# Kernel tuning notes

Measured on AMD Instinct MI355X. Metric: run time of the kernel, lower is better.

The kernel has to match this reference:

```python
import jax, jax.numpy as jnp
import numpy as np

B, N = 16384, 20
F = 128          # n_node_features = n_neighbors_features = embed_dim
T = 100          # time_dim
E = 128          # n_edge_features
H = 2            # n_head
OUT = 128        # output_dimension
KEY_DIM = F + T + E  # 356


def setup_inputs() -> dict:
    key = jax.random.key(0)
    ks = jax.random.split(key, 24)
    s = 0.02
    inp = {
        "src_node_features": jax.random.normal(ks[0], (B, F), jnp.float32),
        "neighbors_features": jax.random.normal(ks[1], (B, N, F), jnp.float32),
        "neighbors_time_features": jax.random.normal(ks[2], (B, N, T), jnp.float32),
        "edge_features": jax.random.normal(ks[3], (B, N, E), jnp.float32),
        "neighbors_padding_mask": jax.random.randint(ks[4], (B, N), 0, 2).astype(bool),
        "weights": jax.random.uniform(ks[5], (B, N), jnp.float32),
        # transform: Linear(key_dim -> F)
        "Wt": jax.random.normal(ks[6], (F, KEY_DIM), jnp.float32) * s,
        "bt": jnp.zeros((F,), jnp.float32),
        # MultiheadAttention projections (embed_dim = kdim = vdim = F)
        "Wq": jax.random.normal(ks[7], (F, F), jnp.float32) * s,
        "bq": jnp.zeros((F,), jnp.float32),
        "Wk": jax.random.normal(ks[8], (F, F), jnp.float32) * s,
        "bk": jnp.zeros((F,), jnp.float32),
        "Wv": jax.random.normal(ks[9], (F, F), jnp.float32) * s,
        "bv": jnp.zeros((F,), jnp.float32),
        "Wo": jax.random.normal(ks[10], (F, F), jnp.float32) * s,
        "bo": jnp.zeros((F,), jnp.float32),
        # MergeLayer: fc1(query_dim + F -> F), fc2(F -> OUT)
        "W1": jax.random.normal(ks[11], (F, F + F), jnp.float32) * s,
        "b1": jnp.zeros((F,), jnp.float32),
        "W2": jax.random.normal(ks[12], (OUT, F), jnp.float32) * s,
        "b2": jnp.zeros((OUT,), jnp.float32),
    }
    return inp


def _gat_forward(src, nbr, timef, edgef, w, mask,
                 Wt, bt, Wq, bq, Wk, bk, Wv, bv, Wo, bo, W1, b1, W2, b2):
    b, f = src.shape
    dh = f // H
    scale = 1.0 / jnp.sqrt(jnp.asarray(dh, src.dtype))
    # key = transform(cat([nbr, edge, time])) * weights  -> [B,N,F]
    k_in = jnp.concatenate([nbr, edgef, timef], axis=2)
    keyv = (jnp.einsum('bnk,fk->bnf', k_in, Wt) + bt) * w[:, :, None]
    # invalid-neighborhood fixup: rows fully padded get their first slot unmasked
    invalid = mask.all(axis=1, keepdims=True)           # [B,1]
    mask = mask.at[:, 0].set(jnp.where(invalid[:, 0], False, mask[:, 0]))
    # projections (query_len = 1)
    q = (src @ Wq.T + bq).reshape(b, H, dh)             # [B,H,dh]
    k = (keyv @ Wk.T + bk).reshape(b, N, H, dh)         # [B,N,H,dh]
    v = (keyv @ Wv.T + bv).reshape(b, N, H, dh)
    scores = jnp.einsum('bhd,bnhd->bhn', q, k) * scale  # [B,H,N]
    scores = jnp.where(mask[:, None, :], -jnp.inf, scores)
    attn = jax.nn.softmax(scores, axis=-1)
    ctx = jnp.einsum('bhn,bnhd->bhd', attn, v).reshape(b, f)
    out = ctx @ Wo.T + bo                               # [B,F]
    out = jnp.where(invalid, jnp.asarray(0.0, out.dtype), out)
    out = jax.nn.relu(out)
    # MergeLayer: fc2(relu(fc1(cat([attn_out, src]))))
    hmid = jax.nn.relu(jnp.concatenate([out, src], axis=1) @ W1.T + b1)
    return hmid @ W2.T + b2


def reference(src_node_features, neighbors_features, neighbors_time_features,
              edge_features, neighbors_padding_mask, weights,
              Wt, bt, Wq, bq, Wk, bk, Wv, bv, Wo, bo, W1, b1, W2, b2):
    return _gat_forward(src_node_features, neighbors_features,
                        neighbors_time_features, edge_features, weights,
                        neighbors_padding_mask,
                        Wt, bt, Wq, bq, Wk, bk, Wv, bv, Wo, bo, W1, b1, W2, b2)
```

## Files before the change

kernel.cpp:

```cpp
#include <hip/hip_runtime.h>
#include <math.h>

#define NN 20
#define FF 128
#define TT 100
#define EE 128
#define KD 356

typedef unsigned int u32;
typedef unsigned short u16;
typedef unsigned long long u64;
typedef __attribute__((ext_vector_type(4))) float f32x4;
typedef __attribute__((ext_vector_type(8))) short s16x8;
typedef __attribute__((ext_vector_type(4))) u32 u32x4;

__device__ __forceinline__ u16 f2b(float f) {
    u32 u = __float_as_uint(f);
    u32 r = u + 0x7FFFu + ((u >> 16) & 1u);
    return (u16)(r >> 16);
}
__device__ __forceinline__ float b2f(u16 h) { return __uint_as_float(((u32)h) << 16); }
__device__ __forceinline__ float blo(u32 u){ return __uint_as_float(u << 16); }
__device__ __forceinline__ float bhi(u32 u){ return __uint_as_float(u & 0xFFFF0000u); }
__device__ __forceinline__ u32 pk2(float a, float b){ return (u32)f2b(a) | ((u32)f2b(b) << 16); }
__device__ __forceinline__ u32 cvtpk(float a, float b){
    u32 d; asm("v_cvt_pk_bf16_f32 %0, %1, %2" : "=v"(d) : "v"(a), "v"(b)); return d;
}


__global__ void prep_fuse(const float* __restrict__ Wt, const float* __restrict__ bt,
                          const float* __restrict__ Wk, const float* __restrict__ Wv,
                          const u32* __restrict__ maskw,
                          float* __restrict__ wkt, float* __restrict__ wvt,
                          float* __restrict__ kfb, float* __restrict__ vfb, int* __restrict__ flagp)
{
    const int blk = blockIdx.x, t = threadIdx.x;
    if (blk < KD) {
        __shared__ float col[FF];
        col[t] = Wt[t * KD + blk];
        __syncthreads();
        float ak = 0.f, av = 0.f;
        for (int j = 0; j < FF; ++j) {
            float c = col[j];
            ak = fmaf(Wk[t * FF + j], c, ak);
            av = fmaf(Wv[t * FF + j], c, av);
        }
        wkt[blk * FF + t] = ak;
        wvt[blk * FF + t] = av;
    } else if (blk == KD) {
        float ak = 0.f, av = 0.f;
        for (int j = 0; j < FF; ++j) {
            float c = bt[j];
            ak = fmaf(Wk[t * FF + j], c, ak);
            av = fmaf(Wv[t * FF + j], c, av);
        }
        kfb[t] = ak; vfb[t] = av;
    } else {
        int any = 0;
        for (int i = t; i < 8192; i += 128) any |= (maskw[i] > 1u) ? 1 : 0;
        any = __any(any) ? 1 : 0;
        __shared__ int red[2];
        if ((t & 63) == 0) red[t >> 6] = any;
        __syncthreads();
        if (t == 0) *flagp = (red[0] | red[1]) ? 1 : 0;
    }
}

__global__ void prep_pack_v4(const float* __restrict__ wkt, const float* __restrict__ wvt,
                             const float* __restrict__ Wq, const float* __restrict__ Wo,
                             const float* __restrict__ W1, const float* __restrict__ W2,
                             u16* __restrict__ kvB, u16* __restrict__ wqI, u16* __restrict__ woI,
                             u16* __restrict__ w1I, u16* __restrict__ w2I)
{
    const int id = blockIdx.x * 256 + threadIdx.x;
    if (id < 196608) {
        int chunk = id >> 9, e = id & 511;
        int ln = e >> 3, ee = e & 7;
        int kt = chunk >> 4, nb = chunk & 15;
        int k = kt * 32 + (ln >> 4) * 8 + ee;
        int n = nb * 16 + (ln & 15);
        float v = 0.f;
        if (k < KD) v = (n < FF) ? wkt[k * FF + n] : wvt[k * FF + (n - FF)];
        kvB[id] = f2b(v);
    } else if (id < 215040) {
        int e = id - 196608; int rem = e % 9216;
        int n = rem / 72, kk = rem % 72; int k = (e / 9216) * 64 + kk;
        wqI[e] = f2b(kk < 64 ? Wq[n * FF + k] : 0.f);
    } else if (id < 233472) {
        int e = id - 215040; int rem = e % 9216;
        int n = rem / 72, kk = rem % 72; int k = (e / 9216) * 64 + kk;
        woI[e] = f2b(kk < 64 ? Wo[n * FF + k] : 0.f);
    } else if (id < 270336) {
        int e = id - 233472; int rem = e % 9216;
        int n = rem / 72, kk = rem % 72; int k = (e / 9216) * 64 + kk;
        w1I[e] = f2b(kk < 64 ? W1[n * 2 * FF + k] : 0.f);
    } else if (id < 288768) {
        int e = id - 270336; int rem = e % 9216;
        int n = rem / 72, kk = rem % 72; int k = (e / 9216) * 64 + kk;
        w2I[e] = f2b(kk < 64 ? W2[n * FF + k] : 0.f);
    }
}

__global__ __launch_bounds__(512) void kv_attn_fused7(
    const float* __restrict__ nbr, const float* __restrict__ edg, const float* __restrict__ tmf,
    const float* __restrict__ wgt, const float* __restrict__ bk, const float* __restrict__ bv,
    const u16* __restrict__ kvB, const float* __restrict__ kfb, const float* __restrict__ vfb,
    const u16* __restrict__ Qg, const void* __restrict__ maskp, const int* __restrict__ flagp,
    u16* __restrict__ ctxout, unsigned char* __restrict__ flags)
{
    __shared__ __align__(16) u16 smem[15680];
    char* sb = (char*)smem;
    float* p_lds = (float*)(sb + 30720);
    u16* kls = (u16*)sb;

    const int tid = threadIdx.x;
    const int lane = tid & 63, wave = tid >> 6;
    const int wn = wave;
    const int Mbase = blockIdx.x * 80;
    const int Bbase = blockIdx.x * 4;
    const int kg = lane >> 4, l16 = lane & 15;

    f32x4 acc[5][2] = {};
    s16x8 br[2][2];
    f32x4 tl[5];

    #define STAGE_CHUNK(C, KT) do {                                                         \
        int row_ = (C) * 8 + (lane >> 3);                                                   \
        int x_ = (lane & 7) ^ (row_ & 7);                                                   \
        const float* g_;                                                                    \
        if ((KT) < 4)      g_ = nbr + (size_t)(Mbase + row_) * 128 + (KT) * 32 + x_ * 4;    \
        else if ((KT) < 8) g_ = edg + (size_t)(Mbase + row_) * 128 + ((KT)-4) * 32 + x_ * 4;\
        else               g_ = tmf + (size_t)(Mbase + row_) * 100 + ((KT)-8) * 32 + x_ * 4;\
        __builtin_amdgcn_global_load_lds((const __attribute__((address_space(1))) u32*)g_,  \
            (__attribute__((address_space(3))) u32*)(sb + ((KT)%3)*10240 + (C)*1024), 16, 0, 0); \
    } while (0)

    #define STAGE(KT) do {                                                                  \
        STAGE_CHUNK(wave, KT);                                                              \
        if (wave < 2) STAGE_CHUNK(8 + wave, KT);                                            \
    } while (0)

    #define LOADB(KT) do {                                                                  \
        br[(KT)&1][0] = *(const s16x8*)(kvB + (size_t)((KT)*16 + wn*2 + 0)*512 + lane*8);   \
        br[(KT)&1][1] = *(const s16x8*)(kvB + (size_t)((KT)*16 + wn*2 + 1)*512 + lane*8);   \
    } while (0)

    #define NV1(KT) ((KT)==0?6:((KT)==1?8:((KT)==2?10:((KT)<=8?8:((KT)==9?7:6)))))
    #define NV2(KT) ((KT)==0?8:((KT)==1?10:((KT)==2?12:((KT)<=8?10:((KT)==9?8:6)))))

    #pragma unroll
    for (int mt = 0; mt < 5; ++mt)
        tl[mt] = *(const f32x4*)(tmf + (size_t)(Mbase + mt * 16 + l16) * 100 + 96);
    STAGE(0); STAGE(1); STAGE(2);
    LOADB(0); LOADB(1);

    #define GITER(KT) do {                                                                  \
        if ((KT) <= 10) {                                                                   \
            if (wave < 2) { asm volatile("s_waitcnt vmcnt(%0)" :: "i"(NV2(KT)) : "memory"); }\
            else          { asm volatile("s_waitcnt vmcnt(%0)" :: "i"(NV1(KT)) : "memory"); }\
            __builtin_amdgcn_s_barrier();                                                   \
            __builtin_amdgcn_sched_barrier(0);                                              \
        }                                                                                   \
        s16x8 af[5];                                                                        \
        _Pragma("unroll")                                                                   \
        for (int mt = 0; mt < 5; ++mt) {                                                    \
            f32x4 lo, hi;                                                                   \
            if ((KT) <= 10) {                                                               \
                int r_ = mt * 16 + l16; int sw_ = r_ & 7; int y0_ = kg * 2;                 \
                const char* bp_ = sb + ((KT)%3)*10240 + r_ * 128;                           \
                lo = *(const f32x4*)(bp_ + ((y0_ ^ sw_) << 4));                             \
                hi = *(const f32x4*)(bp_ + (((y0_+1) ^ sw_) << 4));                         \
            } else {                                                                        \
                lo = (kg == 0) ? tl[mt] : (f32x4){0.f,0.f,0.f,0.f};                         \
                hi = (f32x4){0.f,0.f,0.f,0.f};                                              \
            }                                                                               \
            u32x4 q_;                                                                       \
            q_.x = cvtpk(lo.x, lo.y); q_.y = cvtpk(lo.z, lo.w);                             \
            q_.z = cvtpk(hi.x, hi.y); q_.w = cvtpk(hi.z, hi.w);                             \
            af[mt] = __builtin_bit_cast(s16x8, q_);                                         \
        }                                                                                   \
        _Pragma("unroll")                                                                   \
        for (int mt = 0; mt < 5; ++mt) {                                                    \
            acc[mt][0] = __builtin_amdgcn_mfma_f32_16x16x32_bf16(af[mt], br[(KT)&1][0], acc[mt][0], 0, 0, 0); \
            acc[mt][1] = __builtin_amdgcn_mfma_f32_16x16x32_bf16(af[mt], br[(KT)&1][1], acc[mt][1], 0, 0, 0); \
        }                                                                                   \
        if ((KT) <= 10) {                                                                   \
            asm volatile("s_waitcnt lgkmcnt(0)" ::: "memory");                              \
            __builtin_amdgcn_s_barrier();                                                   \
            __builtin_amdgcn_sched_barrier(0);                                              \
            if ((KT) <= 7) STAGE((KT)+3);                                                   \
            if ((KT)+2 <= 11) LOADB((KT)+2);                                                \
        }                                                                                   \
    } while (0)

    GITER(0); GITER(1); GITER(2);  GITER(3);
    GITER(4); GITER(5); GITER(6);  GITER(7);
    GITER(8); GITER(9); GITER(10); GITER(11);
    #undef GITER
    #undef STAGE
    #undef STAGE_CHUNK
    #undef LOADB

    __syncthreads();

    const int rg4 = (lane >> 4) * 4;
    if (wn < 4) {
        #pragma unroll
        for (int mt = 0; mt < 5; ++mt) {
            const int r0 = mt * 16 + rg4;
            float w4v[4];
            #pragma unroll
            for (int i = 0; i < 4; ++i) w4v[i] = wgt[Mbase + r0 + i];
            #pragma unroll
            for (int nt = 0; nt < 2; ++nt) {
                const int c = wn * 32 + nt * 16 + l16;
                const float fb = kfb[c], bb = bk[c];
                #pragma unroll
                for (int i = 0; i < 4; ++i)
                    kls[(r0 + i) * 132 + c] = f2b(fmaf(acc[mt][nt][i] + fb, w4v[i], bb));
            }
        }
    } else {
        #pragma unroll
        for (int mt = 0; mt < 5; ++mt) {
            const int r0 = mt * 16 + rg4;
            float w4v[4];
            #pragma unroll
            for (int i = 0; i < 4; ++i) w4v[i] = wgt[Mbase + r0 + i];
            #pragma unroll
            for (int nt = 0; nt < 2; ++nt) {
                const int c = (wn - 4) * 32 + nt * 16 + l16;
                const float fb = vfb[c], bb = bv[c];
                #pragma unroll
                for (int i = 0; i < 4; ++i)
                    acc[mt][nt][i] = fmaf(acc[mt][nt][i] + fb, w4v[i], bb);
            }
        }
    }
    __syncthreads();

    const int lb = wave >> 1, h = wave & 1;
    const int brow = Bbase + lb;
    {
        const int flagv = *flagp;
        bool mybit = false;
        if (lane < NN) {
            if (flagv) mybit = ((const unsigned char*)maskp)[brow * NN + lane] != 0;
            else       mybit = ((const int*)maskp)[brow * NN + lane] != 0;
        }
        u64 bal = __ballot(mybit);
        u32 mb = (u32)(bal & 0xFFFFFull);
        const bool invalid = (mb == 0xFFFFFu);
        if (invalid) mb &= ~1u;
        if (h == 0 && lane == 0) flags[brow] = invalid ? 1 : 0;

        const int n = lane & 31;
        float s = -INFINITY;
        if (lane < 32 && n < NN) {
            const u16* kr = kls + (lb * NN + n) * 132 + h * 64;
            const u16* qr = Qg + (size_t)brow * 128 + h * 64;
            float d = 0.f;
            #pragma unroll
            for (int dc = 0; dc < 16; ++dc) {
                uint2 kw = *(const uint2*)(kr + dc * 4);
                uint2 qw = *(const uint2*)(qr + dc * 4);
                d = fmaf(blo(kw.x), blo(qw.x), d);  d = fmaf(bhi(kw.x), bhi(qw.x), d);
                d = fmaf(blo(kw.y), blo(qw.y), d);  d = fmaf(bhi(kw.y), bhi(qw.y), d);
            }
            s = ((mb >> n) & 1u) ? -INFINITY : d * 0.125f;
        }
        float mx = s;
        #pragma unroll
        for (int off = 16; off; off >>= 1) mx = fmaxf(mx, __shfl_xor(mx, off, 32));
        float e = (lane < 32 && n < NN) ? expf(s - mx) : 0.f;
        float sum = e;
        #pragma unroll
        for (int off = 16; off; off >>= 1) sum += __shfl_xor(sum, off, 32);
        if (lane < NN) p_lds[wave * NN + lane] = e / sum;
    }
    __syncthreads();

    if (wn >= 4) {
        #pragma unroll
        for (int mt = 0; mt < 5; ++mt) {
            const int r0 = mt * 16 + rg4;
            #pragma unroll
            for (int nt = 0; nt < 2; ++nt) {
                const int c = (wn - 4) * 32 + nt * 16 + l16;
                #pragma unroll
                for (int i = 0; i < 4; ++i)
                    kls[(r0 + i) * 132 + c] = f2b(acc[mt][nt][i]);
            }
        }
    }
    __syncthreads();

    {
        float cacc = 0.f;
        #pragma unroll
        for (int n2 = 0; n2 < NN; ++n2) {
            float pn = p_lds[wave * NN + n2];
            cacc = fmaf(pn, b2f(kls[(lb * NN + n2) * 132 + h * 64 + lane]), cacc);
        }
        ctxout[(size_t)brow * 128 + h * 64 + lane] = f2b(cacc);
    }
}

#define GM_Q 0
#define GM_O 1
#define GM_H 2
#define GM_F 3

template<int MODE>
__global__ __launch_bounds__(256) void gemm_small(
    const void* __restrict__ Asrc, const float* __restrict__ Asrc2,
    const u16* __restrict__ Bimg, const float* __restrict__ bias,
    const unsigned char* __restrict__ flags, void* __restrict__ outp)
{
    __shared__ u16 lA[64 * 72];
    __shared__ u16 lB[128 * 72];
    const int tid = threadIdx.x;
    const int Mbase = blockIdx.x * 64;
    const int lane = tid & 63, wave = tid >> 6;
    const int wm = wave >> 1, wn = wave & 1;
    const int row = tid >> 2, cg = tid & 3;

    constexpr int KTILES = (MODE == GM_H) ? 4 : 2;
    f32x4 acc[2][4] = {};
    const size_t r = (size_t)(Mbase + row);

    for (int kt = 0; kt < KTILES; ++kt) {
        if (MODE == GM_Q || (MODE == GM_H && kt >= 2)) {
            const float* ap = (MODE == GM_Q)
                ? ((const float*)Asrc + r * 128 + kt * 64 + cg * 16)
                : (Asrc2 + r * 128 + (kt - 2) * 64 + cg * 16);
            f32x4 x0 = *(const f32x4*)ap,       x1 = *(const f32x4*)(ap + 4);
            f32x4 x2 = *(const f32x4*)(ap + 8), x3 = *(const f32x4*)(ap + 12);
            *(uint4*)(&lA[row * 72 + cg * 16])     = make_uint4(pk2(x0.x,x0.y), pk2(x0.z,x0.w), pk2(x1.x,x1.y), pk2(x1.z,x1.w));
            *(uint4*)(&lA[row * 72 + cg * 16 + 8]) = make_uint4(pk2(x2.x,x2.y), pk2(x2.z,x2.w), pk2(x3.x,x3.y), pk2(x3.z,x3.w));
        } else {
            const u16* ap = (const u16*)Asrc + r * 128 + kt * 64 + cg * 16;
            *(uint4*)(&lA[row * 72 + cg * 16])     = *(const uint4*)ap;
            *(uint4*)(&lA[row * 72 + cg * 16 + 8]) = *(const uint4*)(ap + 8);
        }
        for (int c = wave; c < 18; c += 4) {
            const char* g = (const char*)Bimg + (size_t)kt * 18432 + c * 1024 + lane * 16;
            char* l = (char*)lB + c * 1024;
            __builtin_amdgcn_global_load_lds((const __attribute__((address_space(1))) u32*)g,
                                             (__attribute__((address_space(3))) u32*)l, 16, 0, 0);
        }
        __syncthreads();
        #pragma unroll
        for (int ks = 0; ks < 2; ++ks) {
            int kk = ks * 32 + (lane >> 4) * 8;
            s16x8 a[2], b[4];
            #pragma unroll
            for (int mt = 0; mt < 2; ++mt)
                a[mt] = *(const s16x8*)(&lA[(wm * 32 + mt * 16 + (lane & 15)) * 72 + kk]);
            #pragma unroll
            for (int nt = 0; nt < 4; ++nt)
                b[nt] = *(const s16x8*)(&lB[(wn * 64 + nt * 16 + (lane & 15)) * 72 + kk]);
            #pragma unroll
            for (int mt = 0; mt < 2; ++mt)
                #pragma unroll
                for (int nt = 0; nt < 4; ++nt)
                    acc[mt][nt] = __builtin_amdgcn_mfma_f32_16x16x32_bf16(a[mt], b[nt], acc[mt][nt], 0, 0, 0);
        }
        __syncthreads();
    }

    #pragma unroll
    for (int mt = 0; mt < 2; ++mt) {
        #pragma unroll
        for (int nt = 0; nt < 4; ++nt) {
            int colg = wn * 64 + nt * 16 + (lane & 15);
            float bb = bias[colg];
            #pragma unroll
            for (int i = 0; i < 4; ++i) {
                int rg = Mbase + wm * 32 + mt * 16 + (lane >> 4) * 4 + i;
                float val = acc[mt][nt][i] + bb;
                if (MODE == GM_O) { if (flags[rg]) val = 0.f; val = fmaxf(val, 0.f); }
                if (MODE == GM_H) val = fmaxf(val, 0.f);
                if (MODE == GM_F) ((float*)outp)[(size_t)rg * 128 + colg] = val;
                else              ((u16*)outp)[(size_t)rg * 128 + colg] = f2b(val);
            }
        }
    }
}


__global__ void prep_pack_r2(const float* __restrict__ wkt, const float* __restrict__ wvt,
                             const float* __restrict__ Wq, const float* __restrict__ Wo,
                             const float* __restrict__ W1, const float* __restrict__ W2,
                             u16* __restrict__ bpack, u32* __restrict__ wq2, u32* __restrict__ wo2,
                             u32* __restrict__ w12, u32* __restrict__ w22)
{
    const int id = blockIdx.x * 256 + threadIdx.x;
    if (id < 98304) {
        int kt = id >> 14;
        int o  = id & 16383;
        int n  = o >> 6;
        int kk = (o & 63) ^ ((n & 7) << 3);
        int k  = kt * 64 + kk;
        float v = 0.f;
        if (k < KD) v = (n < FF) ? wkt[k * FF + n] : wvt[k * FF + (n - FF)];
        bpack[id] = f2b(v);
    } else if (id < 106496) {
        int e = id - 98304; int j = e >> 6, tt = e & 63;
        wq2[e] = (u32)f2b(Wq[tt * FF + j]) | ((u32)f2b(Wq[(tt + 64) * FF + j]) << 16);
    } else if (id < 114688) {
        int e = id - 106496; int j = e >> 6, tt = e & 63;
        wo2[e] = (u32)f2b(Wo[tt * FF + j]) | ((u32)f2b(Wo[(tt + 64) * FF + j]) << 16);
    } else if (id < 131072) {
        int e = id - 114688; int j = e >> 6, tt = e & 63;
        w12[e] = (u32)f2b(W1[tt * 2 * FF + j]) | ((u32)f2b(W1[(tt + 64) * 2 * FF + j]) << 16);
    } else if (id < 139264) {
        int e = id - 131072; int j = e >> 6, tt = e & 63;
        w22[e] = (u32)f2b(W2[tt * FF + j]) | ((u32)f2b(W2[(tt + 64) * FF + j]) << 16);
    }
}

__global__ __launch_bounds__(512) void kv_gemm_r2(
    const float* __restrict__ nbr, const float* __restrict__ edg, const float* __restrict__ tmf,
    const float* __restrict__ wgt, const float* __restrict__ bk, const float* __restrict__ bv,
    const u16* __restrict__ bpack, const float* __restrict__ kfb, const float* __restrict__ vfb,
    u16* __restrict__ kvout)
{
    __shared__ u16 lA[128 * 64];
    __shared__ u16 lB[256 * 64];
    const int tid = threadIdx.x;
    const int Mbase = blockIdx.x * 128;
    const int lane = tid & 63, wave = tid >> 6;
    const int wm = wave >> 2, wn = wave & 3;

    f32x4 acc[4][4] = {};
    const int rq = tid >> 4;
    const int cq = tid & 15;

    for (int kt = 0; kt < 6; ++kt) {
        #pragma unroll
        for (int i = 0; i < 4; ++i) {
            int row = rq + i * 32;
            size_t r = (size_t)(Mbase + row);
            f32x4 v;
            if (kt < 2)       v = *(const f32x4*)(nbr + r * 128 + kt * 64 + cq * 4);
            else if (kt < 4)  v = *(const f32x4*)(edg + r * 128 + (kt - 2) * 64 + cq * 4);
            else if (kt == 4) v = *(const f32x4*)(tmf + r * 100 + cq * 4);
            else if (cq < 9)  v = *(const f32x4*)(tmf + r * 100 + 64 + cq * 4);
            else              v = (f32x4){0.f, 0.f, 0.f, 0.f};
            int off = row * 64 + ((cq * 4) ^ ((row & 7) << 3));
            *(uint2*)(&lA[off]) = make_uint2(pk2(v.x, v.y), pk2(v.z, v.w));
        }
        #pragma unroll
        for (int i = 0; i < 4; ++i) {
            int boff = wave * 4096 + i * 1024;
            const char* g = (const char*)bpack + (size_t)kt * 32768 + boff + lane * 16;
            char* l = (char*)lB + boff;
            __builtin_amdgcn_global_load_lds((const __attribute__((address_space(1))) u32*)g,
                                             (__attribute__((address_space(3))) u32*)l, 16, 0, 0);
        }
        __syncthreads();
        #pragma unroll
        for (int ks = 0; ks < 2; ++ks) {
            int kk = ks * 32 + (lane >> 4) * 8;
            s16x8 a[4], b[4];
            #pragma unroll
            for (int mt = 0; mt < 4; ++mt) {
                int m = wm * 64 + mt * 16 + (lane & 15);
                a[mt] = *(const s16x8*)(&lA[m * 64 + (kk ^ ((m & 7) << 3))]);
            }
            #pragma unroll
            for (int nt = 0; nt < 4; ++nt) {
                int n = wn * 64 + nt * 16 + (lane & 15);
                b[nt] = *(const s16x8*)(&lB[n * 64 + (kk ^ ((n & 7) << 3))]);
            }
            #pragma unroll
            for (int mt = 0; mt < 4; ++mt)
                #pragma unroll
                for (int nt = 0; nt < 4; ++nt)
                    acc[mt][nt] = __builtin_amdgcn_mfma_f32_16x16x32_bf16(a[mt], b[nt], acc[mt][nt], 0, 0, 0);
        }
        __syncthreads();
    }

    #pragma unroll
    for (int mt = 0; mt < 4; ++mt) {
        float w4[4];
        #pragma unroll
        for (int i = 0; i < 4; ++i)
            w4[i] = wgt[Mbase + wm * 64 + mt * 16 + (lane >> 4) * 4 + i];
        #pragma unroll
        for (int nt = 0; nt < 4; ++nt) {
            int c = wn * 64 + nt * 16 + (lane & 15);
            float fb   = (c < FF) ? kfb[c] : vfb[c - FF];
            float bias = (c < FF) ? bk[c]  : bv[c - FF];
            #pragma unroll
            for (int i = 0; i < 4; ++i) {
                int rr = Mbase + wm * 64 + mt * 16 + (lane >> 4) * 4 + i;
                float val = fmaf(acc[mt][nt][i] + fb, w4[i], bias);
                kvout[(size_t)rr * 256 + c] = f2b(val);
            }
        }
    }
}

__global__ __launch_bounds__(64) void gat_attn_r2(
    const float* __restrict__ src, const void* __restrict__ maskp,
    const float* __restrict__ bq, const float* __restrict__ bo,
    const float* __restrict__ b1, const float* __restrict__ b2,
    const u16* __restrict__ kv, const u32* __restrict__ wq2, const u32* __restrict__ wo2,
    const u32* __restrict__ w12, const u32* __restrict__ w22,
    const int* __restrict__ flagp, float* __restrict__ out)
{
    const int b = blockIdx.x, t = threadIdx.x;
    __shared__ u16 kls[NN * 132];
    __shared__ float s_src[FF], s_q[FF], s_ctx[FF], s_out[FF], s_h[FF];
    __shared__ float s_sc[2 * NN];

    const int flag = *flagp;
    bool mybit = false;
    if (t < NN) {
        if (flag) mybit = ((const unsigned char*)maskp)[b * NN + t] != 0;
        else      mybit = ((const int*)maskp)[b * NN + t] != 0;
    }
    u64 bal = __ballot(mybit);
    u32 mb = (u32)(bal & 0xFFFFFull);
    const bool invalid = (mb == 0xFFFFFu);
    if (invalid) mb &= ~1u;

    s_src[t] = src[(size_t)b * FF + t];
    s_src[t + 64] = src[(size_t)b * FF + 64 + t];

    float v0[NN], v1[NN];
    #pragma unroll
    for (int n = 0; n < NN; ++n) {
        const u16* row = kv + ((size_t)b * NN + n) * 256;
        kls[n * 132 + t]      = row[t];
        kls[n * 132 + 64 + t] = row[64 + t];
        v0[n] = b2f(row[128 + t]);
        v1[n] = b2f(row[192 + t]);
    }
    __syncthreads();

    {
        float q0 = bq[t], q1 = bq[64 + t];
        for (int j = 0; j < FF; ++j) {
            u32 u = wq2[j * 64 + t];
            float sj = s_src[j];
            q0 = fmaf(blo(u), sj, q0);
            q1 = fmaf(bhi(u), sj, q1);
        }
        s_q[t] = q0; s_q[64 + t] = q1;
    }
    __syncthreads();

    if (t < 2 * NN) {
        int h = t / NN, n = t - (t / NN) * NN;
        const u16* kr = kls + n * 132 + h * 64;
        const float* qr = s_q + h * 64;
        float s = 0.f;
        #pragma unroll
        for (int d = 0; d < 64; ++d) s = fmaf(qr[d], b2f(kr[d]), s);
        s *= 0.125f;
        s_sc[t] = ((mb >> n) & 1u) ? -INFINITY : s;
    }
    __syncthreads();
    if (t < 2) {
        float mx = -INFINITY;
        for (int n = 0; n < NN; ++n) mx = fmaxf(mx, s_sc[t * NN + n]);
        float e[NN]; float sum = 0.f;
        for (int n = 0; n < NN; ++n) { e[n] = expf(s_sc[t * NN + n] - mx); sum += e[n]; }
        float inv = 1.f / sum;
        for (int n = 0; n < NN; ++n) s_sc[t * NN + n] = e[n] * inv;
    }
    __syncthreads();

    {
        float c0 = 0.f, c1 = 0.f;
        #pragma unroll
        for (int n = 0; n < NN; ++n) {
            c0 = fmaf(s_sc[n],      v0[n], c0);
            c1 = fmaf(s_sc[NN + n], v1[n], c1);
        }
        s_ctx[t] = c0; s_ctx[64 + t] = c1;
    }
    __syncthreads();

    {
        float o0 = bo[t], o1 = bo[64 + t];
        for (int j = 0; j < FF; ++j) {
            u32 u = wo2[j * 64 + t];
            float cj = s_ctx[j];
            o0 = fmaf(blo(u), cj, o0);
            o1 = fmaf(bhi(u), cj, o1);
        }
        if (invalid) { o0 = 0.f; o1 = 0.f; }
        o0 = fmaxf(o0, 0.f); o1 = fmaxf(o1, 0.f);
        s_out[t] = o0; s_out[64 + t] = o1;
    }
    __syncthreads();

    {
        float h0 = b1[t], h1 = b1[64 + t];
        for (int j = 0; j < FF; ++j) {
            u32 u = w12[j * 64 + t];
            float xj = s_out[j];
            h0 = fmaf(blo(u), xj, h0);
            h1 = fmaf(bhi(u), xj, h1);
        }
        for (int j = 0; j < FF; ++j) {
            u32 u = w12[(FF + j) * 64 + t];
            float xj = s_src[j];
            h0 = fmaf(blo(u), xj, h0);
            h1 = fmaf(bhi(u), xj, h1);
        }
        h0 = fmaxf(h0, 0.f); h1 = fmaxf(h1, 0.f);
        s_h[t] = h0; s_h[64 + t] = h1;
    }
    __syncthreads();

    {
        float f0 = b2[t], f1 = b2[64 + t];
        for (int j = 0; j < FF; ++j) {
            u32 u = w22[j * 64 + t];
            float hj = s_h[j];
            f0 = fmaf(blo(u), hj, f0);
            f1 = fmaf(bhi(u), hj, f1);
        }
        out[(size_t)b * FF + t] = f0;
        out[(size_t)b * FF + 64 + t] = f1;
    }
}


#define FB_WKT  0
#define FB_WVT  (FB_WKT + KD*FF)
#define FB_KB   (FB_WVT + KD*FF)
#define FB_VB   (FB_KB + FF)
#define FB_WQT  (FB_VB + FF)
#define FB_WOT  (FB_WQT + FF*FF)
#define FB_W1T  (FB_WOT + FF*FF)
#define FB_W2T  (FB_W1T + 2*FF*FF)
#define FB_FLAG (FB_W2T + FF*FF)

__global__ void gat_prep_fb(const float* __restrict__ Wt, const float* __restrict__ bt,
                            const float* __restrict__ Wq, const float* __restrict__ Wk,
                            const float* __restrict__ Wv, const float* __restrict__ Wo,
                            const float* __restrict__ W1, const float* __restrict__ W2,
                            const u32* __restrict__ maskw, float* __restrict__ ws)
{
    const int blk = blockIdx.x;
    const int t = threadIdx.x;
    if (blk < KD) {
        __shared__ float col[FF];
        col[t] = Wt[t * KD + blk];
        __syncthreads();
        float ak = 0.f, av = 0.f;
        for (int j = 0; j < FF; ++j) {
            float c = col[j];
            ak = fmaf(Wk[t * FF + j], c, ak);
            av = fmaf(Wv[t * FF + j], c, av);
        }
        ws[FB_WKT + blk * FF + t] = ak;
        ws[FB_WVT + blk * FF + t] = av;
    } else if (blk == KD) {
        float ak = 0.f, av = 0.f;
        for (int j = 0; j < FF; ++j) {
            float c = bt[j];
            ak = fmaf(Wk[t * FF + j], c, ak);
            av = fmaf(Wv[t * FF + j], c, av);
        }
        ws[FB_KB + t] = ak;
        ws[FB_VB + t] = av;
    } else if (blk == KD + 1) {
        int any = 0;
        for (int i = t; i < 8192; i += 128) any |= (maskw[i] > 1u) ? 1 : 0;
        any = __any(any) ? 1 : 0;
        __shared__ int red[2];
        if ((t & 63) == 0) red[t >> 6] = any;
        __syncthreads();
        if (t == 0) ((int*)ws)[FB_FLAG] = (red[0] | red[1]) ? 1 : 0;
    } else {
        int id = (blk - (KD + 2)) * 128 + t;
        if (id < FF * FF) {
            int k = id >> 7, f = id & 127;
            ws[FB_WQT + id] = Wq[f * FF + k];
        } else if (id < 2 * FF * FF) {
            int e = id - FF * FF; int k = e >> 7, f = e & 127;
            ws[FB_WOT + e] = Wo[f * FF + k];
        } else if (id < 4 * FF * FF) {
            int e = id - 2 * FF * FF; int j = e >> 7, f = e & 127;
            ws[FB_W1T + e] = W1[f * (2 * FF) + j];
        } else if (id < 5 * FF * FF) {
            int e = id - 4 * FF * FF; int k = e >> 7, f = e & 127;
            ws[FB_W2T + e] = W2[f * FF + k];
        }
    }
}

__global__ __launch_bounds__(64) void gat_main_fb(
    const float* __restrict__ src, const float* __restrict__ nbr,
    const float* __restrict__ tmf, const float* __restrict__ edg,
    const void* __restrict__ maskp, const float* __restrict__ wgt,
    const float* __restrict__ bq, const float* __restrict__ bk,
    const float* __restrict__ bv, const float* __restrict__ bo,
    const float* __restrict__ b1, const float* __restrict__ b2,
    const float* __restrict__ ws, float* __restrict__ out)
{
    const int b = blockIdx.x;
    const int t = threadIdx.x;
    __shared__ __align__(16) float kin[KD * NN];
    __shared__ float s_src[FF], s_q[FF], s_ctx[FF], s_out[FF], s_h[FF];
    __shared__ float s_w[NN], s_sc[2 * NN];

    const int flag = ((const int*)ws)[FB_FLAG];
    bool mybit = false;
    if (t < NN) {
        if (flag) mybit = ((const unsigned char*)maskp)[b * NN + t] != 0;
        else      mybit = ((const int*)maskp)[b * NN + t] != 0;
    }
    u64 bal = __ballot(mybit);
    u32 mb = (u32)(bal & 0xFFFFFull);
    const bool invalid = (mb == 0xFFFFFu);
    if (invalid) mb &= ~1u;

    s_src[t] = src[(size_t)b * FF + t];
    s_src[t + 64] = src[(size_t)b * FF + 64 + t];
    if (t < NN) s_w[t] = wgt[(size_t)b * NN + t];

    for (int idx = t; idx < NN * FF; idx += 64) {
        int n = idx >> 7, j = idx & 127;
        kin[j * NN + n]         = nbr[((size_t)b * NN + n) * FF + j];
        kin[(128 + j) * NN + n] = edg[((size_t)b * NN + n) * EE + j];
    }
    for (int idx = t; idx < NN * TT; idx += 64) {
        int n = idx / TT, j = idx - n * TT;
        kin[(256 + j) * NN + n] = tmf[((size_t)b * NN + n) * TT + j];
    }
    __syncthreads();

    const float* wkt = ws + FB_WKT;
    const float* wvt = ws + FB_WVT;
    float ak0[NN], ak1[NN], av0[NN], av1[NN];
#pragma unroll
    for (int n = 0; n < NN; ++n) { ak0[n] = 0.f; ak1[n] = 0.f; av0[n] = 0.f; av1[n] = 0.f; }
    for (int k = 0; k < KD; ++k) {
        float wk0 = wkt[k * FF + t],      wk1 = wkt[k * FF + 64 + t];
        float wv0 = wvt[k * FF + t],      wv1 = wvt[k * FF + 64 + t];
        const float4* cp = (const float4*)(kin + k * NN);
        float4 ca = cp[0], cb = cp[1], cc = cp[2], cd = cp[3], ce = cp[4];
        const float c[NN] = { ca.x, ca.y, ca.z, ca.w,  cb.x, cb.y, cb.z, cb.w,
                              cc.x, cc.y, cc.z, cc.w,  cd.x, cd.y, cd.z, cd.w,
                              ce.x, ce.y, ce.z, ce.w };
#pragma unroll
        for (int n = 0; n < NN; ++n) {
            ak0[n] = fmaf(wk0, c[n], ak0[n]);
            ak1[n] = fmaf(wk1, c[n], ak1[n]);
            av0[n] = fmaf(wv0, c[n], av0[n]);
            av1[n] = fmaf(wv1, c[n], av1[n]);
        }
    }
    __syncthreads();

    float* kls = kin;
    float* vls = kin + NN * 129;
    {
        const float kb0 = ws[FB_KB + t], kb1 = ws[FB_KB + 64 + t];
        const float vb0 = ws[FB_VB + t], vb1 = ws[FB_VB + 64 + t];
        const float k0b = bk[t], k1b = bk[64 + t];
        const float v0b = bv[t], v1b = bv[64 + t];
#pragma unroll
        for (int n = 0; n < NN; ++n) {
            float wn = s_w[n];
            kls[n * 129 + t]      = fmaf(wn, ak0[n] + kb0, k0b);
            kls[n * 129 + 64 + t] = fmaf(wn, ak1[n] + kb1, k1b);
            vls[n * 129 + t]      = fmaf(wn, av0[n] + vb0, v0b);
            vls[n * 129 + 64 + t] = fmaf(wn, av1[n] + vb1, v1b);
        }
    }
    {
        const float* wqT = ws + FB_WQT;
        float q0 = bq[t], q1 = bq[64 + t];
        for (int j = 0; j < FF; ++j) {
            float sj = s_src[j];
            q0 = fmaf(wqT[j * FF + t], sj, q0);
            q1 = fmaf(wqT[j * FF + 64 + t], sj, q1);
        }
        s_q[t] = q0; s_q[64 + t] = q1;
    }
    __syncthreads();

    if (t < 2 * NN) {
        int h = t / NN, n = t - (t / NN) * NN;
        const float* kr = kls + n * 129 + h * 64;
        const float* qr = s_q + h * 64;
        float s = 0.f;
#pragma unroll
        for (int d = 0; d < 64; ++d) s = fmaf(qr[d], kr[d], s);
        s *= 0.125f;
        s_sc[t] = ((mb >> n) & 1u) ? -INFINITY : s;
    }
    __syncthreads();
    if (t < 2) {
        float mx = -INFINITY;
        for (int n = 0; n < NN; ++n) mx = fmaxf(mx, s_sc[t * NN + n]);
        float e[NN]; float sum = 0.f;
        for (int n = 0; n < NN; ++n) { e[n] = expf(s_sc[t * NN + n] - mx); sum += e[n]; }
        float inv = 1.f / sum;
        for (int n = 0; n < NN; ++n) s_sc[t * NN + n] = e[n] * inv;
    }
    __syncthreads();

    {
        float c0 = 0.f, c1 = 0.f;
#pragma unroll
        for (int n = 0; n < NN; ++n) {
            c0 = fmaf(s_sc[n],      vls[n * 129 + t],      c0);
            c1 = fmaf(s_sc[NN + n], vls[n * 129 + 64 + t], c1);
        }
        s_ctx[t] = c0; s_ctx[64 + t] = c1;
    }
    __syncthreads();

    {
        const float* woT = ws + FB_WOT;
        float o0 = bo[t], o1 = bo[64 + t];
        for (int j = 0; j < FF; ++j) {
            float cj = s_ctx[j];
            o0 = fmaf(woT[j * FF + t], cj, o0);
            o1 = fmaf(woT[j * FF + 64 + t], cj, o1);
        }
        if (invalid) { o0 = 0.f; o1 = 0.f; }
        o0 = fmaxf(o0, 0.f); o1 = fmaxf(o1, 0.f);
        s_out[t] = o0; s_out[64 + t] = o1;
    }
    __syncthreads();

    {
        const float* w1T = ws + FB_W1T;
        float h0 = b1[t], h1 = b1[64 + t];
        for (int j = 0; j < FF; ++j) {
            float xj = s_out[j];
            h0 = fmaf(w1T[j * FF + t], xj, h0);
            h1 = fmaf(w1T[j * FF + 64 + t], xj, h1);
        }
        for (int j = 0; j < FF; ++j) {
            float xj = s_src[j];
            h0 = fmaf(w1T[(FF + j) * FF + t], xj, h0);
            h1 = fmaf(w1T[(FF + j) * FF + 64 + t], xj, h1);
        }
        h0 = fmaxf(h0, 0.f); h1 = fmaxf(h1, 0.f);
        s_h[t] = h0; s_h[64 + t] = h1;
    }
    __syncthreads();

    {
        const float* w2T = ws + FB_W2T;
        float f0 = b2[t], f1 = b2[64 + t];
        for (int j = 0; j < FF; ++j) {
            float hj = s_h[j];
            f0 = fmaf(w2T[j * FF + t], hj, f0);
            f1 = fmaf(w2T[j * FF + 64 + t], hj, f1);
        }
        out[(size_t)b * FF + t] = f0;
        out[(size_t)b * FF + 64 + t] = f1;
    }
}


extern "C" void kernel_launch(void* const* d_in, const int* in_sizes, int n_in,
                              void* d_out, int out_size, void* d_ws, size_t ws_size,
                              hipStream_t stream)
{
    const float* src = (const float*)d_in[0];
    const float* nbr = (const float*)d_in[1];
    const float* tmf = (const float*)d_in[2];
    const float* edg = (const float*)d_in[3];
    const void*  msk = d_in[4];
    const float* wgt = (const float*)d_in[5];
    const float* Wt  = (const float*)d_in[6];
    const float* bt  = (const float*)d_in[7];
    const float* Wq  = (const float*)d_in[8];
    const float* bq  = (const float*)d_in[9];
    const float* Wk  = (const float*)d_in[10];
    const float* bk  = (const float*)d_in[11];
    const float* Wv  = (const float*)d_in[12];
    const float* bv  = (const float*)d_in[13];
    const float* Wo  = (const float*)d_in[14];
    const float* bo  = (const float*)d_in[15];
    const float* W1  = (const float*)d_in[16];
    const float* b1  = (const float*)d_in[17];
    const float* W2  = (const float*)d_in[18];
    const float* b2  = (const float*)d_in[19];

    const int B = in_sizes[0] / FF;
    const size_t M = (size_t)B * NN;

    size_t o1 = 0;
    size_t t1_qa   = o1; o1 += (size_t)B * 256;
    size_t t1_ch   = o1; o1 += (size_t)B * 256;
    size_t t1_kvB  = o1; o1 += 393216;
    size_t t1_wqI  = o1; o1 += 36864;
    size_t t1_woI  = o1; o1 += 36864;
    size_t t1_w1I  = o1; o1 += 73728;
    size_t t1_w2I  = o1; o1 += 36864;
    size_t t1_wkt  = o1; o1 += (size_t)KD * FF * 4;
    size_t t1_wvt  = o1; o1 += (size_t)KD * FF * 4;
    size_t t1_kfb  = o1; o1 += 512;
    size_t t1_vfb  = o1; o1 += 512;
    size_t t1_flg  = o1; o1 += (size_t)B;
    o1 = (o1 + 255) & ~(size_t)255;
    size_t t1_flag = o1; o1 += 64;
    const size_t need1 = o1;

    size_t o2 = 0;
    size_t t2_kv    = o2; o2 += M * 512;
    size_t t2_bpack = o2; o2 += 98304ull * 2;
    size_t t2_wkt   = o2; o2 += (size_t)KD * FF * 4;
    size_t t2_wvt   = o2; o2 += (size_t)KD * FF * 4;
    size_t t2_kfb   = o2; o2 += 512;
    size_t t2_vfb   = o2; o2 += 512;
    size_t t2_wq2   = o2; o2 += 32768;
    size_t t2_wo2   = o2; o2 += 32768;
    size_t t2_w12   = o2; o2 += 65536;
    size_t t2_w22   = o2; o2 += 32768;
    size_t t2_flag  = o2; o2 += 64;
    const size_t need2 = o2;

    char* w = (char*)d_ws;

    if (ws_size >= need1 && (B % 64) == 0) {
        u16*   qa    = (u16*)(w + t1_qa);
        u16*   ch    = (u16*)(w + t1_ch);
        u16*   kvB   = (u16*)(w + t1_kvB);
        u16*   wqI   = (u16*)(w + t1_wqI);
        u16*   woI   = (u16*)(w + t1_woI);
        u16*   w1I   = (u16*)(w + t1_w1I);
        u16*   w2I   = (u16*)(w + t1_w2I);
        float* wktp  = (float*)(w + t1_wkt);
        float* wvtp  = (float*)(w + t1_wvt);
        float* kfb   = (float*)(w + t1_kfb);
        float* vfb   = (float*)(w + t1_vfb);
        unsigned char* flg = (unsigned char*)(w + t1_flg);
        int*   flagp = (int*)(w + t1_flag);

        prep_fuse<<<dim3(KD + 2), dim3(128), 0, stream>>>(Wt, bt, Wk, Wv,
            (const u32*)msk, wktp, wvtp, kfb, vfb, flagp);
        prep_pack_v4<<<dim3(1128), dim3(256), 0, stream>>>(wktp, wvtp, Wq, Wo, W1, W2,
            kvB, wqI, woI, w1I, w2I);
        gemm_small<GM_Q><<<dim3(B / 64), dim3(256), 0, stream>>>(
            (const void*)src, nullptr, wqI, bq, nullptr, (void*)qa);
        kv_attn_fused7<<<dim3(B / 4), dim3(512), 0, stream>>>(
            nbr, edg, tmf, wgt, bk, bv, kvB, kfb, vfb, qa, msk, flagp, ch, flg);
        gemm_small<GM_O><<<dim3(B / 64), dim3(256), 0, stream>>>(
            (const void*)ch, nullptr, woI, bo, flg, (void*)qa);
        gemm_small<GM_H><<<dim3(B / 64), dim3(256), 0, stream>>>(
            (const void*)qa, src, w1I, b1, nullptr, (void*)ch);
        gemm_small<GM_F><<<dim3(B / 64), dim3(256), 0, stream>>>(
            (const void*)ch, nullptr, w2I, b2, nullptr, d_out);
    } else if (ws_size >= need2 && (M % 128) == 0) {
        u16*   kvp   = (u16*)(w + t2_kv);
        u16*   bpack = (u16*)(w + t2_bpack);
        float* wktp  = (float*)(w + t2_wkt);
        float* wvtp  = (float*)(w + t2_wvt);
        float* kfb   = (float*)(w + t2_kfb);
        float* vfb   = (float*)(w + t2_vfb);
        u32*   wq2   = (u32*)(w + t2_wq2);
        u32*   wo2   = (u32*)(w + t2_wo2);
        u32*   w12   = (u32*)(w + t2_w12);
        u32*   w22   = (u32*)(w + t2_w22);
        int*   flagp = (int*)(w + t2_flag);

        prep_fuse<<<dim3(KD + 2), dim3(128), 0, stream>>>(Wt, bt, Wk, Wv,
            (const u32*)msk, wktp, wvtp, kfb, vfb, flagp);
        prep_pack_r2<<<dim3(544), dim3(256), 0, stream>>>(wktp, wvtp, Wq, Wo, W1, W2,
            bpack, wq2, wo2, w12, w22);
        kv_gemm_r2<<<dim3((int)(M / 128)), dim3(512), 0, stream>>>(
            nbr, edg, tmf, wgt, bk, bv, bpack, kfb, vfb, kvp);
        gat_attn_r2<<<dim3(B), dim3(64), 0, stream>>>(
            src, msk, bq, bo, b1, b2, kvp, wq2, wo2, w12, w22, flagp, (float*)d_out);
    } else {
        float* ws = (float*)d_ws;
        gat_prep_fb<<<dim3(KD + 2 + 640), dim3(128), 0, stream>>>(
            Wt, bt, Wq, Wk, Wv, Wo, W1, W2, (const u32*)msk, ws);
        gat_main_fb<<<dim3(B), dim3(64), 0, stream>>>(
            src, nbr, tmf, edg, msk, wgt, bq, bk, bv, bo, b1, b2, ws, (float*)d_out);
    }
}
```

Before: 207.6 us.

## Fuse output projection and MergeLayer GEMMs into one tail kernel

Replaces the three separate small GEMM launches (Wo projection with mask/relu, fc1 over concat with src, fc2) with a single kernel. Each 64-row block keeps its intermediate activations in LDS as bf16 instead of writing them to global memory and reading them back. This removes two kernel launches and the global round-trips for the intermediates. The cost is extra LDS per block (an added 64x136 buffer), which may lower occupancy, and the three GEMM phases now run back to back with more synchronisation inside one block.

```diff
diff --git a/kernel.cpp b/kernel.cpp
--- a/kernel.cpp
+++ b/kernel.cpp
@@ -307,9 +307,6 @@
 }
 
 #define GM_Q 0
-#define GM_O 1
-#define GM_H 2
-#define GM_F 3
 
 template<int MODE>
 __global__ __launch_bounds__(256) void gemm_small(
@@ -325,23 +322,16 @@
     const int wm = wave >> 1, wn = wave & 1;
     const int row = tid >> 2, cg = tid & 3;
 
-    constexpr int KTILES = (MODE == GM_H) ? 4 : 2;
     f32x4 acc[2][4] = {};
     const size_t r = (size_t)(Mbase + row);
 
-    for (int kt = 0; kt < KTILES; ++kt) {
-        if (MODE == GM_Q || (MODE == GM_H && kt >= 2)) {
-            const float* ap = (MODE == GM_Q)
-                ? ((const float*)Asrc + r * 128 + kt * 64 + cg * 16)
-                : (Asrc2 + r * 128 + (kt - 2) * 64 + cg * 16);
+    for (int kt = 0; kt < 2; ++kt) {
+        {
+            const float* ap = (const float*)Asrc + r * 128 + kt * 64 + cg * 16;
             f32x4 x0 = *(const f32x4*)ap,       x1 = *(const f32x4*)(ap + 4);
             f32x4 x2 = *(const f32x4*)(ap + 8), x3 = *(const f32x4*)(ap + 12);
             *(uint4*)(&lA[row * 72 + cg * 16])     = make_uint4(pk2(x0.x,x0.y), pk2(x0.z,x0.w), pk2(x1.x,x1.y), pk2(x1.z,x1.w));
             *(uint4*)(&lA[row * 72 + cg * 16 + 8]) = make_uint4(pk2(x2.x,x2.y), pk2(x2.z,x2.w), pk2(x3.x,x3.y), pk2(x3.z,x3.w));
-        } else {
-            const u16* ap = (const u16*)Asrc + r * 128 + kt * 64 + cg * 16;
-            *(uint4*)(&lA[row * 72 + cg * 16])     = *(const uint4*)ap;
-            *(uint4*)(&lA[row * 72 + cg * 16 + 8]) = *(const uint4*)(ap + 8);
         }
         for (int c = wave; c < 18; c += 4) {
             const char* g = (const char*)Bimg + (size_t)kt * 18432 + c * 1024 + lane * 16;
@@ -378,14 +368,151 @@
             #pragma unroll
             for (int i = 0; i < 4; ++i) {
                 int rg = Mbase + wm * 32 + mt * 16 + (lane >> 4) * 4 + i;
+                ((u16*)outp)[(size_t)rg * 128 + colg] = f2b(acc[mt][nt][i] + bb);
+            }
+        }
+    }
+}
+
+__global__ __launch_bounds__(256) void gemm_tail(
+    const u16* __restrict__ ctx, const float* __restrict__ src,
+    const u16* __restrict__ woI, const u16* __restrict__ w1I, const u16* __restrict__ w2I,
+    const float* __restrict__ bo, const float* __restrict__ b1, const float* __restrict__ b2,
+    const unsigned char* __restrict__ flags, float* __restrict__ outp)
+{
+    __shared__ u16 lA[64 * 72];
+    __shared__ u16 lB[128 * 72];
+    __shared__ u16 s_a[64 * 136];
+    const int tid = threadIdx.x;
+    const int Mbase = blockIdx.x * 64;
+    const int lane = tid & 63, wave = tid >> 6;
+    const int wm = wave >> 1, wn = wave & 1;
+    const int row = tid >> 2, cg = tid & 3;
+    const size_t r = (size_t)(Mbase + row);
+
+    #define STAGEB(IMG, KT) do {                                                            \
+        for (int c_ = wave; c_ < 18; c_ += 4) {                                             \
+            const char* g_ = (const char*)(IMG) + (size_t)(KT) * 18432 + c_ * 1024 + lane * 16; \
+            char* l_ = (char*)lB + c_ * 1024;                                               \
+            __builtin_amdgcn_global_load_lds((const __attribute__((address_space(1))) u32*)g_, \
+                                             (__attribute__((address_space(3))) u32*)l_, 16, 0, 0); \
+        }                                                                                   \
+    } while (0)
+
+    #define MFMA_STEP(ASRC, ASTRIDE, KOFF) do {                                             \
+        _Pragma("unroll")                                                                   \
+        for (int ks_ = 0; ks_ < 2; ++ks_) {                                                 \
+            int kk_ = ks_ * 32 + (lane >> 4) * 8;                                           \
+            s16x8 a_[2], b_[4];                                                             \
+            _Pragma("unroll")                                                               \
+            for (int mt_ = 0; mt_ < 2; ++mt_)                                               \
+                a_[mt_] = *(const s16x8*)(&(ASRC)[(wm * 32 + mt_ * 16 + (lane & 15)) * (ASTRIDE) + (KOFF) + kk_]); \
+            _Pragma("unroll")                                                               \
+            for (int nt_ = 0; nt_ < 4; ++nt_)                                               \
+                b_[nt_] = *(const s16x8*)(&lB[(wn * 64 + nt_ * 16 + (lane & 15)) * 72 + kk_]); \
+            _Pragma("unroll")                                                               \
+            for (int mt_ = 0; mt_ < 2; ++mt_)                                               \
+                _Pragma("unroll")                                                           \
+                for (int nt_ = 0; nt_ < 4; ++nt_)                                           \
+                    acc[mt_][nt_] = __builtin_amdgcn_mfma_f32_16x16x32_bf16(a_[mt_], b_[nt_], acc[mt_][nt_], 0, 0, 0); \
+        }                                                                                   \
+    } while (0)
+
+    f32x4 acc[2][4];
+
+    #pragma unroll
+    for (int mt = 0; mt < 2; ++mt)
+        #pragma unroll
+        for (int nt = 0; nt < 4; ++nt) acc[mt][nt] = (f32x4){0.f,0.f,0.f,0.f};
+
+    for (int kt = 0; kt < 2; ++kt) {
+        {
+            const u16* ap = ctx + r * 128 + kt * 64 + cg * 16;
+            *(uint4*)(&lA[row * 72 + cg * 16])     = *(const uint4*)ap;
+            *(uint4*)(&lA[row * 72 + cg * 16 + 8]) = *(const uint4*)(ap + 8);
+        }
+        STAGEB(woI, kt);
+        __syncthreads();
+        MFMA_STEP(lA, 72, 0);
+        __syncthreads();
+    }
+    #pragma unroll
+    for (int mt = 0; mt < 2; ++mt) {
+        #pragma unroll
+        for (int nt = 0; nt < 4; ++nt) {
+            int colg = wn * 64 + nt * 16 + (lane & 15);
+            float bb = bo[colg];
+            #pragma unroll
+            for (int i = 0; i < 4; ++i) {
+                int rl = wm * 32 + mt * 16 + (lane >> 4) * 4 + i;
                 float val = acc[mt][nt][i] + bb;
-                if (MODE == GM_O) { if (flags[rg]) val = 0.f; val = fmaxf(val, 0.f); }
-                if (MODE == GM_H) val = fmaxf(val, 0.f);
-                if (MODE == GM_F) ((float*)outp)[(size_t)rg * 128 + colg] = val;
-                else              ((u16*)outp)[(size_t)rg * 128 + colg] = f2b(val);
+                if (flags[Mbase + rl]) val = 0.f;
+                s_a[rl * 136 + colg] = f2b(fmaxf(val, 0.f));
             }
         }
     }
+    __syncthreads();
+
+    #pragma unroll
+    for (int mt = 0; mt < 2; ++mt)
+        #pragma unroll
+        for (int nt = 0; nt < 4; ++nt) acc[mt][nt] = (f32x4){0.f,0.f,0.f,0.f};
+
+    for (int kt = 0; kt < 4; ++kt) {
+        if (kt >= 2) {
+            const float* ap = src + r * 128 + (kt - 2) * 64 + cg * 16;
+            f32x4 x0 = *(const f32x4*)ap,       x1 = *(const f32x4*)(ap + 4);
+            f32x4 x2 = *(const f32x4*)(ap + 8), x3 = *(const f32x4*)(ap + 12);
+            *(uint4*)(&lA[row * 72 + cg * 16])     = make_uint4(pk2(x0.x,x0.y), pk2(x0.z,x0.w), pk2(x1.x,x1.y), pk2(x1.z,x1.w));
+            *(uint4*)(&lA[row * 72 + cg * 16 + 8]) = make_uint4(pk2(x2.x,x2.y), pk2(x2.z,x2.w), pk2(x3.x,x3.y), pk2(x3.z,x3.w));
+        }
+        STAGEB(w1I, kt);
+        __syncthreads();
+        if (kt < 2) MFMA_STEP(s_a, 136, kt * 64);
+        else        MFMA_STEP(lA, 72, 0);
+        __syncthreads();
+    }
+    #pragma unroll
+    for (int mt = 0; mt < 2; ++mt) {
+        #pragma unroll
+        for (int nt = 0; nt < 4; ++nt) {
+            int colg = wn * 64 + nt * 16 + (lane & 15);
+            float bb = b1[colg];
+            #pragma unroll
+            for (int i = 0; i < 4; ++i) {
+                int rl = wm * 32 + mt * 16 + (lane >> 4) * 4 + i;
+                s_a[rl * 136 + colg] = f2b(fmaxf(acc[mt][nt][i] + bb, 0.f));
+            }
+        }
+    }
+    __syncthreads();
+
+    #pragma unroll
+    for (int mt = 0; mt < 2; ++mt)
+        #pragma unroll
+        for (int nt = 0; nt < 4; ++nt) acc[mt][nt] = (f32x4){0.f,0.f,0.f,0.f};
+
+    for (int kt = 0; kt < 2; ++kt) {
+        STAGEB(w2I, kt);
+        __syncthreads();
+        MFMA_STEP(s_a, 136, kt * 64);
+        __syncthreads();
+    }
+    #pragma unroll
+    for (int mt = 0; mt < 2; ++mt) {
+        #pragma unroll
+        for (int nt = 0; nt < 4; ++nt) {
+            int colg = wn * 64 + nt * 16 + (lane & 15);
+            float bb = b2[colg];
+            #pragma unroll
+            for (int i = 0; i < 4; ++i) {
+                int rg = Mbase + wm * 32 + mt * 16 + (lane >> 4) * 4 + i;
+                outp[(size_t)rg * 128 + colg] = acc[mt][nt][i] + bb;
+            }
+        }
+    }
+    #undef STAGEB
+    #undef MFMA_STEP
 }
 
 
@@ -952,12 +1079,8 @@
             (const void*)src, nullptr, wqI, bq, nullptr, (void*)qa);
         kv_attn_fused7<<<dim3(B / 4), dim3(512), 0, stream>>>(
             nbr, edg, tmf, wgt, bk, bv, kvB, kfb, vfb, qa, msk, flagp, ch, flg);
-        gemm_small<GM_O><<<dim3(B / 64), dim3(256), 0, stream>>>(
-            (const void*)ch, nullptr, woI, bo, flg, (void*)qa);
-        gemm_small<GM_H><<<dim3(B / 64), dim3(256), 0, stream>>>(
-            (const void*)qa, src, w1I, b1, nullptr, (void*)ch);
-        gemm_small<GM_F><<<dim3(B / 64), dim3(256), 0, stream>>>(
-            (const void*)ch, nullptr, w2I, b2, nullptr, d_out);
+        gemm_tail<<<dim3(B / 64), dim3(256), 0, stream>>>(
+            ch, src, woI, w1I, w2I, bo, b1, b2, flg, (float*)d_out);
     } else if (ws_size >= need2 && (M % 128) == 0) {
         u16*   kvp   = (u16*)(w + t2_kv);
         u16*   bpack = (u16*)(w + t2_bpack);
```

New measurement: 205.2 us. No clear change (-1.2%).
